# Optimization experiments

Measured on AMD Instinct MI355X. Metric: run time of the kernel, lower is better.

The kernel has to match this reference:

```python
import jax, jax.numpy as jnp
import numpy as np

N = 200000        # total nodes
NPL = 12500       # nodes per topological level
NLVL = 16         # number of topological levels (N = NPL*NLVL)
DEG = 8           # avg in-degree for nodes in levels >= 1
IN_DIM = 128
H = 128           # per-direction hidden (unidirectional -> hidden_dim)
LAYERS = 2


def setup_inputs() -> dict:
    rng = np.random.default_rng(0)
    feats = jnp.asarray(rng.standard_normal((N, IN_DIM)).astype(np.float32))
    stdv = 1.0 / np.sqrt(H)
    wx = jnp.asarray(rng.uniform(-stdv, stdv, (IN_DIM + (LAYERS - 1) * H, 1, 3 * H)).astype(np.float32))
    wh = jnp.asarray(rng.uniform(-stdv, stdv, (LAYERS, H, 1, 3 * H)).astype(np.float32))
    b = jnp.asarray(rng.uniform(-stdv, stdv, (LAYERS, 1, 3 * H)).astype(np.float32))
    # DAG edges grouped by destination level; src is any node in an earlier level
    srcs, dsts = [], []
    for lvl in range(1, NLVL):
        dst = np.repeat(np.arange(lvl * NPL, (lvl + 1) * NPL, dtype=np.int32), DEG)
        src = rng.integers(0, lvl * NPL, size=NPL * DEG).astype(np.int32)
        srcs.append(src)
        dsts.append(dst)
    edge_src = jnp.asarray(np.concatenate(srcs))
    edge_dst = jnp.asarray(np.concatenate(dsts))
    index_map = jnp.arange(N, dtype=jnp.int32)
    return dict(features=feats, weights_x=wx, weights_h=wh, biases=b,
                edge_src=edge_src, edge_dst=edge_dst, index_map=index_map,
                num_levels=NLVL, nodes_per_level=NPL)


def _daggru(features, weights_x, weights_h, biases, edge_src, edge_dst,
            index_map, num_levels, nodes_per_level):
    n_nodes, in_dim = features.shape
    layers, hd = weights_h.shape[0], weights_h.shape[1]
    npl = nodes_per_level
    epl = edge_src.shape[0] // (num_levels - 1)  # edges per level block
    # h = zeros.index_add_(0, index_map, features)
    x = jnp.zeros_like(features).at[index_map].add(features)
    row = 0
    h = None
    for layer in range(layers):
        rows = in_dim if layer == 0 else hd
        Wx = weights_x[row:row + rows, 0]          # [rows, 3H]
        row += rows
        Wh = weights_h[layer, :, 0]                # [H, 3H]
        b = biases[layer, 0]                       # [3H]
        gx = x @ Wx + b                            # [N, 3H] precomputed input gates
        h = jnp.zeros((n_nodes, hd), dtype=features.dtype)
        for lvl in range(num_levels):
            s = lvl * npl
            if lvl == 0:
                m = jnp.zeros((npl, hd), dtype=features.dtype)
            else:
                es = edge_src[(lvl - 1) * epl: lvl * epl]
                ed = edge_dst[(lvl - 1) * epl: lvl * epl] - s
                m = jax.ops.segment_sum(h[es], ed, num_segments=npl)
                deg = jax.ops.segment_sum(jnp.ones((epl,), features.dtype), ed, num_segments=npl)
                m = m / jnp.maximum(deg, 1.0)[:, None]   # in-degree normalization
            g = gx[s:s + npl]
            gh = m @ Wh
            r = jax.nn.sigmoid(g[:, :hd] + gh[:, :hd])
            z = jax.nn.sigmoid(g[:, hd:2 * hd] + gh[:, hd:2 * hd])
            n = jnp.tanh(g[:, 2 * hd:] + r * gh[:, 2 * hd:])
            h = h.at[s:s + npl].set((1.0 - z) * n + z * m)
        x = h
    return h[index_map]


def reference(features, weights_x, weights_h, biases, edge_src, edge_dst,
              index_map, num_levels, nodes_per_level):
    return _daggru(features, weights_x, weights_h, biases, edge_src, edge_dst,
                   index_map, num_levels, nodes_per_level)
```

## Files before the change

### kernel.cpp

```cpp
#include <hip/hip_runtime.h>
#include <stdint.h>

#define N_NODES 200000
#define NPL     12500
#define NLVL    16
#define DEG     8
#define EPL     (NPL*DEG)
#define HD      128
#define KTOT    256
#define MT      64
#define NBLK    196
#define ASTR    264
#define WTL     98304

typedef unsigned short u16;
typedef unsigned int   u32;

typedef __attribute__((ext_vector_type(8)))  short  short8;
typedef __attribute__((ext_vector_type(16))) float  f32x16;

__device__ __forceinline__ float bf2f(u32 u) { return __uint_as_float(u << 16); }
__device__ __forceinline__ float bflo(u32 u) { return __uint_as_float(u << 16); }
__device__ __forceinline__ float bfhi(u32 u) { return __uint_as_float(u & 0xFFFF0000u); }
__device__ __forceinline__ u16 f2bf(float f) {
  u32 u = __float_as_uint(f);
  return (u16)((u + 0x7FFFu + ((u >> 16) & 1u)) >> 16);
}
__device__ __forceinline__ u32 pack2(float a, float b) {
  u32 ua = __float_as_uint(a), ub = __float_as_uint(b);
  ua = (ua + 0x7FFFu + ((ua >> 16) & 1u)) >> 16;
  ub = ((ub + 0x7FFFu + ((ub >> 16) & 1u)) >> 16) << 16;
  return ua | ub;
}
__device__ __forceinline__ float fsig(float x) {
  return __builtin_amdgcn_rcpf(1.f + __builtin_amdgcn_exp2f(-1.4426950408889634f * x));
}
__device__ __forceinline__ float ftanh(float x) {
  float t = __builtin_amdgcn_exp2f(2.8853900817779268f * x);
  return 1.f - 2.f * __builtin_amdgcn_rcpf(t + 1.f);
}

__global__ __launch_bounds__(256) void scatter_x(const float* __restrict__ f,
    const int* __restrict__ idx, u16* __restrict__ xb)
{
  const int t = blockIdx.x * 256 + threadIdx.x;
  const int i = t >> 4, sg = (t & 15) * 8;
  const int d = idx[i];
  const float4 a = *(const float4*)(f + (size_t)i * HD + sg);
  const float4 b = *(const float4*)(f + (size_t)i * HD + sg + 4);
  uint4 o;
  o.x = pack2(a.x, a.y); o.y = pack2(a.z, a.w);
  o.z = pack2(b.x, b.y); o.w = pack2(b.z, b.w);
  *(uint4*)(xb + (size_t)d * HD + sg) = o;
}

__global__ __launch_bounds__(256) void gather_out(const u16* __restrict__ hb,
    const int* __restrict__ idx, float* __restrict__ o)
{
  const int t = blockIdx.x * 256 + threadIdx.x;
  const int i = t >> 4, sg = (t & 15) * 8;
  const int s = idx[i];
  const uint4 v = *(const uint4*)(hb + (size_t)s * HD + sg);
  float4 lo, hi;
  lo.x = bflo(v.x); lo.y = bfhi(v.x); lo.z = bflo(v.y); lo.w = bfhi(v.y);
  hi.x = bflo(v.z); hi.y = bfhi(v.z); hi.z = bflo(v.w); hi.w = bfhi(v.w);
  *(float4*)(o + (size_t)i * HD + sg)     = lo;
  *(float4*)(o + (size_t)i * HD + sg + 4) = hi;
}

__global__ __launch_bounds__(256) void build_wt(const float* __restrict__ wx,
    const float* __restrict__ wh, u16* __restrict__ wt)
{
  const int t = blockIdx.x * 256 + threadIdx.x;
  const int l = t / WTL;
  const int r = t - l * WTL;
  const int e = r & 7;
  const int chunk = r >> 3;
  const int lane = chunk & 63;
  const int tile = chunk >> 6;
  const int l31 = lane & 31, lq = lane >> 5;
  int col, k;
  if (tile < 128)      { col =       (tile >> 4) * 32 + l31; k =       (tile & 15) * 16 + lq * 8 + e; }
  else if (tile < 160) { col = 256 + ((tile - 128) >> 3) * 32 + l31; k = ((tile - 128) & 7) * 16 + lq * 8 + e; }
  else                 { col = 384 + ((tile - 160) >> 3) * 32 + l31; k = 128 + ((tile - 160) & 7) * 16 + lq * 8 + e; }
  float v;
  if (col < 384) {
    v = (k < 128) ? wx[(size_t)(l * 128 + k) * 384 + col]
                  : wh[(size_t)l * 49152 + (size_t)(k - 128) * 384 + col];
  } else {
    v = wh[(size_t)l * 49152 + (size_t)(k - 128) * 384 + (col - 128)];
  }
  wt[(size_t)l * WTL + r] = f2bf(v);
}

__global__ __launch_bounds__(256, 2) void level_step(
    u16* __restrict__ bufA, u16* __restrict__ bufB,
    const u16* __restrict__ wt, const float* __restrict__ bias,
    const int* __restrict__ esrc, int stage)
{
  __shared__ __align__(16) u16 sA[MT * ASTR];

  int blk = blockIdx.x, layer, lvl;
  if (blk < NBLK) { layer = 0; lvl = stage; }
  else            { layer = 1; lvl = stage - 1; blk -= NBLK; }
  if (lvl < 0 || lvl >= NLVL) return;

  const u16*   x  = layer ? bufB : bufA;
  u16*         h  = layer ? bufA : bufB;
  const u16*   Wt = wt  + (size_t)layer * WTL;
  const float* bs = bias + (size_t)layer * 384;

  const int tid = threadIdx.x;

  {
    const int sub = tid >> 4;
    const int c8  = (tid & 15) * 8;
    uint4 z4; z4.x = z4.y = z4.z = z4.w = 0u;
    #pragma unroll
    for (int it = 0; it < 4; ++it) {
      const int row  = it * 16 + sub;
      const int lrow = blk * MT + row;
      const bool valid = (lrow < NPL);
      uint4* dx = (uint4*)(sA + row * ASTR + c8);
      *dx = valid ? *(const uint4*)(x + (size_t)(lvl * NPL + lrow) * HD + c8) : z4;
      uint4* dm = (uint4*)(sA + row * ASTR + HD + c8);
      if (lvl > 0 && valid) {
        const int eb = (lvl - 1) * EPL + lrow * DEG;
        const int4 e0 = *(const int4*)(esrc + eb);
        const int4 e1 = *(const int4*)(esrc + eb + 4);
        const int srcs[8] = { e0.x, e0.y, e0.z, e0.w, e1.x, e1.y, e1.z, e1.w };
        float acc[8];
        #pragma unroll
        for (int i = 0; i < 8; ++i) acc[i] = 0.f;
        #pragma unroll
        for (int e = 0; e < 8; ++e) {
          const uint4 v = *(const uint4*)(h + (size_t)srcs[e] * HD + c8);
          acc[0] += bflo(v.x); acc[1] += bfhi(v.x);
          acc[2] += bflo(v.y); acc[3] += bfhi(v.y);
          acc[4] += bflo(v.z); acc[5] += bfhi(v.z);
          acc[6] += bflo(v.w); acc[7] += bfhi(v.w);
        }
        uint4 o;
        o.x = pack2(acc[0] * 0.125f, acc[1] * 0.125f);
        o.y = pack2(acc[2] * 0.125f, acc[3] * 0.125f);
        o.z = pack2(acc[4] * 0.125f, acc[5] * 0.125f);
        o.w = pack2(acc[6] * 0.125f, acc[7] * 0.125f);
        *dm = o;
      } else {
        *dm = z4;
      }
    }
  }
  __syncthreads();

  const int wv = tid >> 6, lane = tid & 63;
  const int l31 = lane & 31, lq = lane >> 5;

  f32x16 acc[2][4];
  {
    const float b0 = bs[      32 * wv + l31];
    const float b1 = bs[128 + 32 * wv + l31];
    const float b2 = bs[256 + 32 * wv + l31];
    #pragma unroll
    for (int r = 0; r < 16; ++r) {
      acc[0][0][r] = b0; acc[1][0][r] = b0;
      acc[0][1][r] = b1; acc[1][1][r] = b1;
      acc[0][2][r] = b2; acc[1][2][r] = b2;
      acc[0][3][r] = 0.f; acc[1][3][r] = 0.f;
    }
  }

  const u16* wlane = Wt + (size_t)lane * 8;
  #pragma unroll
  for (int t = 0; t < 16; ++t) {
    const short8 a0 = *(const short8*)(sA + (l31     ) * ASTR + t * 16 + lq * 8);
    const short8 a1 = *(const short8*)(sA + (32 + l31) * ASTR + t * 16 + lq * 8);
    const short8 b0 = *(const short8*)(wlane + (size_t)((wv    ) * 16 + t) * 512);
    const short8 b1 = *(const short8*)(wlane + (size_t)((wv + 4) * 16 + t) * 512);
    acc[0][0] = __builtin_amdgcn_mfma_f32_32x32x16_bf16(a0, b0, acc[0][0], 0, 0, 0);
    acc[1][0] = __builtin_amdgcn_mfma_f32_32x32x16_bf16(a1, b0, acc[1][0], 0, 0, 0);
    acc[0][1] = __builtin_amdgcn_mfma_f32_32x32x16_bf16(a0, b1, acc[0][1], 0, 0, 0);
    acc[1][1] = __builtin_amdgcn_mfma_f32_32x32x16_bf16(a1, b1, acc[1][1], 0, 0, 0);
    if (t < 8) {
      const short8 b2 = *(const short8*)(wlane + (size_t)(128 + wv * 8 + t) * 512);
      acc[0][2] = __builtin_amdgcn_mfma_f32_32x32x16_bf16(a0, b2, acc[0][2], 0, 0, 0);
      acc[1][2] = __builtin_amdgcn_mfma_f32_32x32x16_bf16(a1, b2, acc[1][2], 0, 0, 0);
    } else {
      const short8 b3 = *(const short8*)(wlane + (size_t)(160 + wv * 8 + (t - 8)) * 512);
      acc[0][3] = __builtin_amdgcn_mfma_f32_32x32x16_bf16(a0, b3, acc[0][3], 0, 0, 0);
      acc[1][3] = __builtin_amdgcn_mfma_f32_32x32x16_bf16(a1, b3, acc[1][3], 0, 0, 0);
    }
  }

  const int jcol = 32 * wv + l31;
  #pragma unroll
  for (int rf = 0; rf < 2; ++rf) {
    #pragma unroll
    for (int r = 0; r < 16; ++r) {
      const int rowe = rf * 32 + (r & 3) + 8 * (r >> 2) + 4 * lq;
      const int lrow = blk * MT + rowe;
      if (lrow < NPL) {
        const float gr  = acc[rf][0][r];
        const float gz  = acc[rf][1][r];
        const float gxn = acc[rf][2][r];
        const float ghn = acc[rf][3][r];
        const float mv  = bf2f(sA[rowe * ASTR + HD + jcol]);
        const float rg  = fsig(gr);
        const float zg  = fsig(gz);
        const float ng  = ftanh(gxn + rg * ghn);
        const float hv  = (1.f - zg) * ng + zg * mv;
        h[(size_t)(lvl * NPL + lrow) * HD + jcol] = f2bf(hv);
      }
    }
  }
}

extern "C" void kernel_launch(void* const* d_in, const int* in_sizes, int n_in,
                              void* d_out, int out_size, void* d_ws, size_t ws_size,
                              hipStream_t stream)
{
  (void)in_sizes; (void)n_in; (void)out_size; (void)ws_size;
  const float* feats = (const float*)d_in[0];
  const float* wx    = (const float*)d_in[1];
  const float* wh    = (const float*)d_in[2];
  const float* bias  = (const float*)d_in[3];
  const int*   esrc  = (const int*)d_in[4];
  const int*   imap  = (const int*)d_in[6];
  float* out = (float*)d_out;

  char* ws = (char*)d_ws;
  u16* bufA = (u16*)ws;
  u16* bufB = (u16*)(ws + 51200000);
  u16* wt   = (u16*)(ws + 102400000);

  scatter_x<<<12500, 256, 0, stream>>>(feats, imap, bufA);
  build_wt<<<768, 256, 0, stream>>>(wx, wh, wt);

  for (int stage = 0; stage <= NLVL; ++stage)
    level_step<<<2 * NBLK, 256, 0, stream>>>(bufA, bufB, wt, bias, esrc, stage);

  gather_out<<<12500, 256, 0, stream>>>(bufA, imap, out);
}
```

Baseline: 644.7 us.

## Fuse per-stage launches into one persistent kernel with atomic grid barrier

Replaces the 17 separate level_step launches with a single persistent level_all kernel that loops over stages. A global atomic counter, reset in build_wt, acts as a grid-wide barrier between stages. The aim is to remove kernel launch and drain overhead between stages. It relies on all 392 blocks being co-resident, or the spin-wait deadlocks, and it adds the cost of atomic polling.

```diff
diff --git a/kernel.cpp b/kernel.cpp
--- a/kernel.cpp
+++ b/kernel.cpp
@@ -10,6 +10,7 @@
 #define KTOT    256
 #define MT      64
 #define NBLK    196
+#define GRID    (2*NBLK)
 #define ASTR    264
 #define WTL     98304
 
@@ -69,9 +70,10 @@
 }
 
 __global__ __launch_bounds__(256) void build_wt(const float* __restrict__ wx,
-    const float* __restrict__ wh, u16* __restrict__ wt)
+    const float* __restrict__ wh, u16* __restrict__ wt, int* __restrict__ done)
 {
   const int t = blockIdx.x * 256 + threadIdx.x;
+  if (t < 4) done[t] = 0;
   const int l = t / WTL;
   const int r = t - l * WTL;
   const int e = r & 7;
@@ -93,17 +95,16 @@
   wt[(size_t)l * WTL + r] = f2bf(v);
 }
 
-__global__ __launch_bounds__(256, 2) void level_step(
+__global__ __launch_bounds__(256, 2) void level_all(
     u16* __restrict__ bufA, u16* __restrict__ bufB,
     const u16* __restrict__ wt, const float* __restrict__ bias,
-    const int* __restrict__ esrc, int stage)
+    const int* __restrict__ esrc, int* done)
 {
   __shared__ __align__(16) u16 sA[MT * ASTR];
 
-  int blk = blockIdx.x, layer, lvl;
-  if (blk < NBLK) { layer = 0; lvl = stage; }
-  else            { layer = 1; lvl = stage - 1; blk -= NBLK; }
-  if (lvl < 0 || lvl >= NLVL) return;
+  const int blk0 = blockIdx.x;
+  const int layer = (blk0 < NBLK) ? 0 : 1;
+  const int blk   = (blk0 < NBLK) ? blk0 : blk0 - NBLK;
 
   const u16*   x  = layer ? bufB : bufA;
   u16*         h  = layer ? bufA : bufB;
@@ -111,107 +112,125 @@
   const float* bs = bias + (size_t)layer * 384;
 
   const int tid = threadIdx.x;
-
-  {
-    const int sub = tid >> 4;
-    const int c8  = (tid & 15) * 8;
-    uint4 z4; z4.x = z4.y = z4.z = z4.w = 0u;
-    #pragma unroll
-    for (int it = 0; it < 4; ++it) {
-      const int row  = it * 16 + sub;
-      const int lrow = blk * MT + row;
-      const bool valid = (lrow < NPL);
-      uint4* dx = (uint4*)(sA + row * ASTR + c8);
-      *dx = valid ? *(const uint4*)(x + (size_t)(lvl * NPL + lrow) * HD + c8) : z4;
-      uint4* dm = (uint4*)(sA + row * ASTR + HD + c8);
-      if (lvl > 0 && valid) {
-        const int eb = (lvl - 1) * EPL + lrow * DEG;
-        const int4 e0 = *(const int4*)(esrc + eb);
-        const int4 e1 = *(const int4*)(esrc + eb + 4);
-        const int srcs[8] = { e0.x, e0.y, e0.z, e0.w, e1.x, e1.y, e1.z, e1.w };
-        float acc[8];
-        #pragma unroll
-        for (int i = 0; i < 8; ++i) acc[i] = 0.f;
-        #pragma unroll
-        for (int e = 0; e < 8; ++e) {
-          const uint4 v = *(const uint4*)(h + (size_t)srcs[e] * HD + c8);
-          acc[0] += bflo(v.x); acc[1] += bfhi(v.x);
-          acc[2] += bflo(v.y); acc[3] += bfhi(v.y);
-          acc[4] += bflo(v.z); acc[5] += bfhi(v.z);
-          acc[6] += bflo(v.w); acc[7] += bfhi(v.w);
-        }
-        uint4 o;
-        o.x = pack2(acc[0] * 0.125f, acc[1] * 0.125f);
-        o.y = pack2(acc[2] * 0.125f, acc[3] * 0.125f);
-        o.z = pack2(acc[4] * 0.125f, acc[5] * 0.125f);
-        o.w = pack2(acc[6] * 0.125f, acc[7] * 0.125f);
-        *dm = o;
-      } else {
-        *dm = z4;
-      }
-    }
-  }
-  __syncthreads();
-
   const int wv = tid >> 6, lane = tid & 63;
   const int l31 = lane & 31, lq = lane >> 5;
 
-  f32x16 acc[2][4];
-  {
-    const float b0 = bs[      32 * wv + l31];
-    const float b1 = bs[128 + 32 * wv + l31];
-    const float b2 = bs[256 + 32 * wv + l31];
-    #pragma unroll
-    for (int r = 0; r < 16; ++r) {
-      acc[0][0][r] = b0; acc[1][0][r] = b0;
-      acc[0][1][r] = b1; acc[1][1][r] = b1;
-      acc[0][2][r] = b2; acc[1][2][r] = b2;
-      acc[0][3][r] = 0.f; acc[1][3][r] = 0.f;
+  const float b0 = bs[      32 * wv + l31];
+  const float b1 = bs[128 + 32 * wv + l31];
+  const float b2 = bs[256 + 32 * wv + l31];
+  const u16* wlane = Wt + (size_t)lane * 8;
+  const int jcol = 32 * wv + l31;
+
+  for (int stage = 0; stage <= NLVL; ++stage) {
+    if (stage > 0) {
+      if (tid == 0) {
+        const int target = GRID * stage;
+        while (__hip_atomic_load(done, __ATOMIC_RELAXED,
+                                 __HIP_MEMORY_SCOPE_AGENT) < target)
+          __builtin_amdgcn_s_sleep(2);
+        __builtin_amdgcn_fence(__ATOMIC_ACQUIRE, "agent");
+      }
+      __syncthreads();
     }
-  }
-
-  const u16* wlane = Wt + (size_t)lane * 8;
-  #pragma unroll
-  for (int t = 0; t < 16; ++t) {
-    const short8 a0 = *(const short8*)(sA + (l31     ) * ASTR + t * 16 + lq * 8);
-    const short8 a1 = *(const short8*)(sA + (32 + l31) * ASTR + t * 16 + lq * 8);
-    const short8 b0 = *(const short8*)(wlane + (size_t)((wv    ) * 16 + t) * 512);
-    const short8 b1 = *(const short8*)(wlane + (size_t)((wv + 4) * 16 + t) * 512);
-    acc[0][0] = __builtin_amdgcn_mfma_f32_32x32x16_bf16(a0, b0, acc[0][0], 0, 0, 0);
-    acc[1][0] = __builtin_amdgcn_mfma_f32_32x32x16_bf16(a1, b0, acc[1][0], 0, 0, 0);
-    acc[0][1] = __builtin_amdgcn_mfma_f32_32x32x16_bf16(a0, b1, acc[0][1], 0, 0, 0);
-    acc[1][1] = __builtin_amdgcn_mfma_f32_32x32x16_bf16(a1, b1, acc[1][1], 0, 0, 0);
-    if (t < 8) {
-      const short8 b2 = *(const short8*)(wlane + (size_t)(128 + wv * 8 + t) * 512);
-      acc[0][2] = __builtin_amdgcn_mfma_f32_32x32x16_bf16(a0, b2, acc[0][2], 0, 0, 0);
-      acc[1][2] = __builtin_amdgcn_mfma_f32_32x32x16_bf16(a1, b2, acc[1][2], 0, 0, 0);
-    } else {
-      const short8 b3 = *(const short8*)(wlane + (size_t)(160 + wv * 8 + (t - 8)) * 512);
-      acc[0][3] = __builtin_amdgcn_mfma_f32_32x32x16_bf16(a0, b3, acc[0][3], 0, 0, 0);
-      acc[1][3] = __builtin_amdgcn_mfma_f32_32x32x16_bf16(a1, b3, acc[1][3], 0, 0, 0);
+
+    const int lvl = stage - layer;
+    if (lvl >= 0 && lvl < NLVL) {
+      {
+        const int sub = tid >> 4;
+        const int c8  = (tid & 15) * 8;
+        uint4 z4; z4.x = z4.y = z4.z = z4.w = 0u;
+        #pragma unroll
+        for (int it = 0; it < 4; ++it) {
+          const int row  = it * 16 + sub;
+          const int lrow = blk * MT + row;
+          const bool valid = (lrow < NPL);
+          uint4* dx = (uint4*)(sA + row * ASTR + c8);
+          *dx = valid ? *(const uint4*)(x + (size_t)(lvl * NPL + lrow) * HD + c8) : z4;
+          uint4* dm = (uint4*)(sA + row * ASTR + HD + c8);
+          if (lvl > 0 && valid) {
+            const int eb = (lvl - 1) * EPL + lrow * DEG;
+            const int4 e0 = *(const int4*)(esrc + eb);
+            const int4 e1 = *(const int4*)(esrc + eb + 4);
+            const int srcs[8] = { e0.x, e0.y, e0.z, e0.w, e1.x, e1.y, e1.z, e1.w };
+            float acc[8];
+            #pragma unroll
+            for (int i = 0; i < 8; ++i) acc[i] = 0.f;
+            #pragma unroll
+            for (int e = 0; e < 8; ++e) {
+              const uint4 v = *(const uint4*)(h + (size_t)srcs[e] * HD + c8);
+              acc[0] += bflo(v.x); acc[1] += bfhi(v.x);
+              acc[2] += bflo(v.y); acc[3] += bfhi(v.y);
+              acc[4] += bflo(v.z); acc[5] += bfhi(v.z);
+              acc[6] += bflo(v.w); acc[7] += bfhi(v.w);
+            }
+            uint4 o;
+            o.x = pack2(acc[0] * 0.125f, acc[1] * 0.125f);
+            o.y = pack2(acc[2] * 0.125f, acc[3] * 0.125f);
+            o.z = pack2(acc[4] * 0.125f, acc[5] * 0.125f);
+            o.w = pack2(acc[6] * 0.125f, acc[7] * 0.125f);
+            *dm = o;
+          } else {
+            *dm = z4;
+          }
+        }
+      }
+      __syncthreads();
+
+      f32x16 acc[2][4];
+      #pragma unroll
+      for (int r = 0; r < 16; ++r) {
+        acc[0][0][r] = b0; acc[1][0][r] = b0;
+        acc[0][1][r] = b1; acc[1][1][r] = b1;
+        acc[0][2][r] = b2; acc[1][2][r] = b2;
+        acc[0][3][r] = 0.f; acc[1][3][r] = 0.f;
+      }
+
+      #pragma unroll
+      for (int t = 0; t < 16; ++t) {
+        const short8 a0 = *(const short8*)(sA + (l31     ) * ASTR + t * 16 + lq * 8);
+        const short8 a1 = *(const short8*)(sA + (32 + l31) * ASTR + t * 16 + lq * 8);
+        const short8 bb0 = *(const short8*)(wlane + (size_t)((wv    ) * 16 + t) * 512);
+        const short8 bb1 = *(const short8*)(wlane + (size_t)((wv + 4) * 16 + t) * 512);
+        acc[0][0] = __builtin_amdgcn_mfma_f32_32x32x16_bf16(a0, bb0, acc[0][0], 0, 0, 0);
+        acc[1][0] = __builtin_amdgcn_mfma_f32_32x32x16_bf16(a1, bb0, acc[1][0], 0, 0, 0);
+        acc[0][1] = __builtin_amdgcn_mfma_f32_32x32x16_bf16(a0, bb1, acc[0][1], 0, 0, 0);
+        acc[1][1] = __builtin_amdgcn_mfma_f32_32x32x16_bf16(a1, bb1, acc[1][1], 0, 0, 0);
+        if (t < 8) {
+          const short8 bb2 = *(const short8*)(wlane + (size_t)(128 + wv * 8 + t) * 512);
+          acc[0][2] = __builtin_amdgcn_mfma_f32_32x32x16_bf16(a0, bb2, acc[0][2], 0, 0, 0);
+          acc[1][2] = __builtin_amdgcn_mfma_f32_32x32x16_bf16(a1, bb2, acc[1][2], 0, 0, 0);
+        } else {
+          const short8 bb3 = *(const short8*)(wlane + (size_t)(160 + wv * 8 + (t - 8)) * 512);
+          acc[0][3] = __builtin_amdgcn_mfma_f32_32x32x16_bf16(a0, bb3, acc[0][3], 0, 0, 0);
+          acc[1][3] = __builtin_amdgcn_mfma_f32_32x32x16_bf16(a1, bb3, acc[1][3], 0, 0, 0);
+        }
+      }
+
+      #pragma unroll
+      for (int rf = 0; rf < 2; ++rf) {
+        #pragma unroll
+        for (int r = 0; r < 16; ++r) {
+          const int rowe = rf * 32 + (r & 3) + 8 * (r >> 2) + 4 * lq;
+          const int lrow = blk * MT + rowe;
+          if (lrow < NPL) {
+            const float gr  = acc[rf][0][r];
+            const float gz  = acc[rf][1][r];
+            const float gxn = acc[rf][2][r];
+            const float ghn = acc[rf][3][r];
+            const float mv  = bf2f(sA[rowe * ASTR + HD + jcol]);
+            const float rg  = fsig(gr);
+            const float zg  = fsig(gz);
+            const float ng  = ftanh(gxn + rg * ghn);
+            const float hv  = (1.f - zg) * ng + zg * mv;
+            h[(size_t)(lvl * NPL + lrow) * HD + jcol] = f2bf(hv);
+          }
+        }
+      }
     }
-  }
-
-  const int jcol = 32 * wv + l31;
-  #pragma unroll
-  for (int rf = 0; rf < 2; ++rf) {
-    #pragma unroll
-    for (int r = 0; r < 16; ++r) {
-      const int rowe = rf * 32 + (r & 3) + 8 * (r >> 2) + 4 * lq;
-      const int lrow = blk * MT + rowe;
-      if (lrow < NPL) {
-        const float gr  = acc[rf][0][r];
-        const float gz  = acc[rf][1][r];
-        const float gxn = acc[rf][2][r];
-        const float ghn = acc[rf][3][r];
-        const float mv  = bf2f(sA[rowe * ASTR + HD + jcol]);
-        const float rg  = fsig(gr);
-        const float zg  = fsig(gz);
-        const float ng  = ftanh(gxn + rg * ghn);
-        const float hv  = (1.f - zg) * ng + zg * mv;
-        h[(size_t)(lvl * NPL + lrow) * HD + jcol] = f2bf(hv);
-      }
-    }
+
+    __syncthreads();
+    if (tid == 0)
+      __hip_atomic_fetch_add(done, 1, __ATOMIC_RELEASE, __HIP_MEMORY_SCOPE_AGENT);
   }
 }
 
@@ -232,12 +251,12 @@
   u16* bufA = (u16*)ws;
   u16* bufB = (u16*)(ws + 51200000);
   u16* wt   = (u16*)(ws + 102400000);
+  int* done = (int*)(ws + 102793216);
 
   scatter_x<<<12500, 256, 0, stream>>>(feats, imap, bufA);
-  build_wt<<<768, 256, 0, stream>>>(wx, wh, wt);
-
-  for (int stage = 0; stage <= NLVL; ++stage)
-    level_step<<<2 * NBLK, 256, 0, stream>>>(bufA, bufB, wt, bias, esrc, stage);
+  build_wt<<<768, 256, 0, stream>>>(wx, wh, wt, done);
+
+  level_all<<<GRID, 256, 0, stream>>>(bufA, bufB, wt, bias, esrc, done);
 
   gather_out<<<12500, 256, 0, stream>>>(bufA, imap, out);
 }
```

Result: slower. 1.186 ms (+84.0%).
